# Kernel tuning notes

Measured on AMD Instinct MI355X. Metric: run time of the kernel, lower is better.

Reference implementation:

```python
import jax, jax.numpy as jnp
import numpy as np

N_HEADS, D_K, D_MODEL = 16, 64, 1024
B, S = 2, 2048


def setup_inputs() -> dict:
    key = jax.random.key(0)
    ks = jax.random.split(key, 9)
    scale = 1.0 / np.sqrt(D_MODEL)
    cscale = 1.0 / np.sqrt(N_HEADS * D_K)
    return {
        "x": jax.random.normal(ks[0], (B, S, D_MODEL), dtype=jnp.float32),
        # per-head projection weights, stacked over heads: [H, d_model, d_k]
        "Wq": jax.random.uniform(ks[1], (N_HEADS, D_MODEL, D_K), jnp.float32, -scale, scale),
        "bq": jax.random.uniform(ks[2], (N_HEADS, D_K), jnp.float32, -scale, scale),
        "Wk": jax.random.uniform(ks[3], (N_HEADS, D_MODEL, D_K), jnp.float32, -scale, scale),
        "bk": jax.random.uniform(ks[4], (N_HEADS, D_K), jnp.float32, -scale, scale),
        "Wv": jax.random.uniform(ks[5], (N_HEADS, D_MODEL, D_K), jnp.float32, -scale, scale),
        "bv": jax.random.uniform(ks[6], (N_HEADS, D_K), jnp.float32, -scale, scale),
        # concat projection: [H*d_k, d_model]
        "Wc": jax.random.uniform(ks[7], (N_HEADS * D_K, D_MODEL), jnp.float32, -cscale, cscale),
        "bc": jax.random.uniform(ks[8], (D_MODEL,), jnp.float32, -cscale, cscale),
    }


def reference(x, Wq, bq, Wk, bk, Wv, bv, Wc, bc):
    # Per-head projections, vectorized across heads: [B,H,S,d_k]
    q = jnp.einsum("bsd,hdk->bhsk", x, Wq) + bq[None, :, None, :]
    k = jnp.einsum("bsd,hdk->bhsk", x, Wk) + bk[None, :, None, :]
    v = jnp.einsum("bsd,hdk->bhsk", x, Wv) + bv[None, :, None, :]
    # scores: [B,H,Sq,Skv]
    scores = jnp.einsum("bhsk,bhtk->bhst", q, k) / jnp.sqrt(jnp.asarray(D_K, x.dtype))
    # FAITHFUL to original: softmax over dim=1 of [B,S,S] = the QUERY axis (axis 2 here)
    attn = jax.nn.softmax(scores, axis=2)
    out = jnp.einsum("bhst,bhtk->bhsk", attn, v)  # [B,H,S,d_k]
    # concat heads along feature dim: [B,S,H*d_k]
    cat = jnp.transpose(out, (0, 2, 1, 3)).reshape(x.shape[0], x.shape[1], -1)
    return cat @ Wc + bc
```

## Files before the change

### kernel.cpp

```cpp
#include <hip/hip_runtime.h>
#include <hip/hip_bf16.h>

#define NH 16
#define DK 64
#define DM 1024
#define BB 2
#define SS 2048
#define BS (BB*SS)

typedef __attribute__((ext_vector_type(8))) short bf16x8;
typedef __attribute__((ext_vector_type(4))) short short4v;
typedef __attribute__((ext_vector_type(4))) float f32x4;

#define MFMA16 __builtin_amdgcn_mfma_f32_16x16x32_bf16

static __device__ __forceinline__ f32x4 MFMA16K16(short4v a, short4v b, f32x4 c) {
#if __has_builtin(__builtin_amdgcn_mfma_f32_16x16x16bf16_1k)
  return __builtin_amdgcn_mfma_f32_16x16x16bf16_1k(a, b, c, 0, 0, 0);
#else
  asm volatile("v_mfma_f32_16x16x16_bf16 %0, %1, %2, %0" : "+v"(c) : "v"(a), "v"(b));
  return c;
#endif
}

#if __has_builtin(__builtin_amdgcn_exp2f)
#define EXP2(x) __builtin_amdgcn_exp2f(x)
#else
#define EXP2(x) __expf((x) * 0.6931471805599453f)
#endif

static __device__ __forceinline__ float bf2f(short s) {
  union { unsigned u; float f; } v;
  v.u = ((unsigned)(unsigned short)s) << 16;
  return v.f;
}
static __device__ __forceinline__ short f2bf(float f) {
  union { float f; unsigned u; } v; v.f = f;
  unsigned r = (v.u + 0x7fffu + ((v.u >> 16) & 1u)) >> 16;
  return (short)r;
}
static __device__ __forceinline__ unsigned pkbf(float a, float b) {
  __hip_bfloat162 h = __float22bfloat162_rn(make_float2(a, b));
  union { __hip_bfloat162 h; unsigned u; } c; c.h = h; return c.u;
}

template<int C16>
static __device__ __forceinline__ int soff(int row, int chunk) {
  return row*(C16*8) + ((chunk ^ (row & (C16-1))) << 3);
}

template<int C16, int R>
static __device__ __forceinline__ void stage(const short* __restrict__ g, int gstride,
                                             short* l, int wave, int lane) {
  const int rloc = lane / C16;
  const int c    = lane % C16;
#pragma unroll
  for (int rr = 0; rr < R; rr += 4*(64/C16)) {
    int rbase = rr + wave*(64/C16);
    int row   = rbase + rloc;
    int cg    = c ^ (row & (C16-1));
    __builtin_amdgcn_global_load_lds(
        (const __attribute__((address_space(1))) void*)(g + (size_t)row*gstride + cg*8),
        (__attribute__((address_space(3))) void*)(l + rbase*(C16*8)),
        16, 0, 0);
  }
}

__global__ __launch_bounds__(256) void k_convert(
    const float* __restrict__ x,
    const float* __restrict__ Wq, const float* __restrict__ Wk,
    const float* __restrict__ Wv, const float* __restrict__ Wc,
    short* __restrict__ xb, short* __restrict__ Wt, short* __restrict__ Wct) {
  __shared__ float T[64][65];
  const int tid = threadIdx.x;
  int bx = blockIdx.x;
  const int XB = BS*DM/(256*4);
  if (bx < XB) {
    int i = (bx*256 + tid)*4;
    float4 v = *(const float4*)&x[i];
    union { unsigned u[2]; short4v s; } o;
    o.u[0] = pkbf(v.x, v.y); o.u[1] = pkbf(v.z, v.w);
    *(short4v*)&xb[i] = o.s;
    return;
  }
  bx -= XB;
  if (bx < 48*16) {
    int th = bx >> 4, d0 = (bx & 15) * 64;
    int type = th >> 4, h = th & 15;
    const float* W = ((type == 0) ? Wq : (type == 1) ? Wk : Wv)
                     + (size_t)h*DM*DK + (size_t)d0*DK;
#pragma unroll
    for (int p = 0; p < 4; p++) {
      int dr = p*16 + (tid >> 4), dkc = (tid & 15) * 4;
      float4 v = *(const float4*)&W[(size_t)dr*DK + dkc];
      T[dkc+0][dr]=v.x; T[dkc+1][dr]=v.y; T[dkc+2][dr]=v.z; T[dkc+3][dr]=v.w;
    }
    __syncthreads();
#pragma unroll
    for (int e = 0; e < 2; e++) {
      int c = tid*2 + e, dk = c >> 3, dd = (c & 7) * 8;
      union { short s[8]; int4 v; } u;
#pragma unroll
      for (int j = 0; j < 8; j++) u.s[j] = f2bf(T[dk][dd+j]);
      *(int4*)&Wt[((size_t)th*DK + dk)*DM + d0 + dd] = u.v;
    }
    return;
  }
  bx -= 48*16;
  int n0 = (bx >> 4) * 64, k0 = (bx & 15) * 64;
#pragma unroll
  for (int p = 0; p < 4; p++) {
    int kr = p*16 + (tid >> 4), nc = (tid & 15) * 4;
    float4 v = *(const float4*)&Wc[(size_t)(k0+kr)*DM + n0 + nc];
    T[nc+0][kr]=v.x; T[nc+1][kr]=v.y; T[nc+2][kr]=v.z; T[nc+3][kr]=v.w;
  }
  __syncthreads();
#pragma unroll
  for (int e = 0; e < 2; e++) {
    int c = tid*2 + e, n = c >> 3, kk = (c & 7) * 8;
    union { short s[8]; int4 v; } u;
#pragma unroll
    for (int j = 0; j < 8; j++) u.s[j] = f2bf(T[n][kk+j]);
    *(int4*)&Wct[(size_t)(n0+n)*DM + k0 + kk] = u.v;
  }
}

__global__ __launch_bounds__(256) void k_qkv(
    const short* __restrict__ xb, const short* __restrict__ Wt,
    const float* __restrict__ bq, const float* __restrict__ bk,
    const float* __restrict__ bv,
    short* __restrict__ Qb, short* __restrict__ Kb, short* __restrict__ Vb) {
  __shared__ __align__(16) short As[128*64];
  __shared__ __align__(16) short Bs[128*64];
  const int tid = threadIdx.x, wave = tid >> 6, lane = tid & 63;
  const int l15 = lane & 15, quad = lane >> 4;
  const int id = blockIdx.x, xcd = id & 7, j = id >> 3;
  const int m0 = (xcd*4 + (j & 3)) * 128, n0 = (j >> 2) * 128;
  const int mw = (wave & 1) * 64, nw = (wave >> 1) * 64;
  f32x4 acc[4][4] = {};
  for (int k0 = 0; k0 < DM; k0 += 64) {
    stage<8,128>(xb + (size_t)m0*DM + k0, DM, As, wave, lane);
    stage<8,128>(Wt + (size_t)n0*DM + k0, DM, Bs, wave, lane);
    __syncthreads();
#pragma unroll
    for (int ks = 0; ks < 2; ks++) {
      bf16x8 a[4], b[4];
#pragma unroll
      for (int g = 0; g < 4; g++)  a[g]  = *(const bf16x8*)&As[soff<8>(mw + g*16 + l15,  ks*4 + quad)];
#pragma unroll
      for (int nf = 0; nf < 4; nf++) b[nf] = *(const bf16x8*)&Bs[soff<8>(nw + nf*16 + l15, ks*4 + quad)];
#pragma unroll
      for (int g = 0; g < 4; g++)
#pragma unroll
        for (int nf = 0; nf < 4; nf++)
          acc[g][nf] = MFMA16(a[g], b[nf], acc[g][nf], 0, 0, 0);
    }
    __syncthreads();
  }
  const int th = (n0 + nw) >> 6;
  const int type = th >> 4, h = th & 15;
  short* dst = (type == 0) ? Qb : (type == 1) ? Kb : Vb;
  const float* bias = ((type == 0) ? bq : (type == 1) ? bk : bv) + h*DK;
  const float scale = (type == 0) ? 0.18033688011112042f : 1.0f;
#pragma unroll
  for (int nf = 0; nf < 4; nf++) {
    int dk = nf*16 + l15;
    float bval = bias[dk];
#pragma unroll
    for (int g = 0; g < 4; g++)
#pragma unroll
      for (int r = 0; r < 4; r++) {
        int m = m0 + mw + g*16 + quad*4 + r;
        int b_ = m >> 11, s = m & (SS-1);
        dst[(size_t)((b_*NH + h)*SS + s)*DK + dk] = f2bf((acc[g][nf][r] + bval) * scale);
      }
  }
}

__global__ __launch_bounds__(256) void k_stats(
    const short* __restrict__ Qb, const short* __restrict__ Kb,
    const short* __restrict__ Vb, short* __restrict__ Vt) {
  __shared__ __align__(16) short smem[3*8192];
  __shared__ float red[4][64];
  __shared__ float zinv[128];
  short* Ks = smem;
  const int tid = threadIdx.x, wave = tid >> 6, lane = tid & 63;
  const int l15 = lane & 15, quad = lane >> 4;
  const int id = blockIdx.x, xcd = id & 7, j = id >> 3;
  const int bh = xcd*4 + (j & 3), t0 = (j >> 2) * 128;
  const short* Qg = Qb + (size_t)bh * SS * DK;
  const short* Kg = Kb + (size_t)bh * SS * DK;
  const int mw = (wave & 1) * 64, nw = (wave >> 1) * 64;
  stage<8,128>(Kg + (size_t)t0*DK, DK, Ks, wave, lane);
  stage<8,128>(Qg, DK, smem + 8192, wave, lane);
  __syncthreads();
  bf16x8 kf[2][4];
#pragma unroll
  for (int ks = 0; ks < 2; ks++)
#pragma unroll
    for (int nf = 0; nf < 4; nf++)
      kf[ks][nf] = *(const bf16x8*)&Ks[soff<8>(nw + nf*16 + l15, ks*4 + quad)];
  float csum[4] = {0.f, 0.f, 0.f, 0.f};
  for (int it = 0; it < SS/128; it++) {
    if (it + 1 < SS/128)
      stage<8,128>(Qg + (size_t)(it+1)*128*DK, DK,
                   smem + 8192 + (((it+1) & 1) << 13), wave, lane);
    const short* Qs = smem + 8192 + ((it & 1) << 13);
    f32x4 acc[4][4] = {};
#pragma unroll
    for (int ks = 0; ks < 2; ks++) {
      bf16x8 a[4];
#pragma unroll
      for (int g = 0; g < 4; g++) a[g] = *(const bf16x8*)&Qs[soff<8>(mw + g*16 + l15, ks*4 + quad)];
#pragma unroll
      for (int g = 0; g < 4; g++)
#pragma unroll
        for (int nf = 0; nf < 4; nf++)
          acc[g][nf] = MFMA16(a[g], kf[ks][nf], acc[g][nf], 0, 0, 0);
    }
#pragma unroll
    for (int nf = 0; nf < 4; nf++)
#pragma unroll
      for (int g = 0; g < 4; g++)
#pragma unroll
        for (int r = 0; r < 4; r++)
          csum[nf] += EXP2(acc[g][nf][r]);
    __syncthreads();
  }
#pragma unroll
  for (int nf = 0; nf < 4; nf++) {
    csum[nf] += __shfl_xor(csum[nf], 16, 64);
    csum[nf] += __shfl_xor(csum[nf], 32, 64);
  }
  if (lane < 16) {
#pragma unroll
    for (int nf = 0; nf < 4; nf++) red[wave][nf*16 + lane] = csum[nf];
  }
  __syncthreads();
  if (tid < 128) {
    int half = tid >> 6, c = tid & 63;
    zinv[tid] = 1.0f / (red[half*2][c] + red[half*2 + 1][c]);
  }
  __syncthreads();
  short* Vtile = smem + 8192;
  const short* Vg = Vb + (size_t)bh * SS * DK;
#pragma unroll
  for (int it = 0; it < 4; it++) {
    int c = tid + it*256;
    int trow = c >> 3, c8 = (c & 7) * 8;
    union { int4 v; short s[8]; } u;
    u.v = *(const int4*)&Vg[(size_t)(t0 + trow)*DK + c8];
    float sc = zinv[trow];
#pragma unroll
    for (int jj = 0; jj < 8; jj++) {
      int dk = c8 + jj;
      Vtile[dk*128 + (((trow >> 3) ^ (dk & 15)) << 3) + (trow & 7)] = f2bf(bf2f(u.s[jj]) * sc);
    }
  }
  __syncthreads();
  short* Vtg = Vt + (size_t)bh * DK * SS;
#pragma unroll
  for (int it = 0; it < 4; it++) {
    int row = it*16 + (tid >> 4), cc = tid & 15;
    *(int4*)&Vtg[(size_t)row*SS + t0 + cc*8] = *(const int4*)&Vtile[soff<16>(row, cc)];
  }
}

__global__ __launch_bounds__(256, 2) void k_attnpv(
    const short* __restrict__ Qb, const short* __restrict__ Kb,
    const short* __restrict__ Vt, short* __restrict__ catg) {
  __shared__ __align__(16) short smem[32768];
  const int tid = threadIdx.x, wave = tid >> 6, lane = tid & 63;
  const int l15 = lane & 15, quad = lane >> 4;
  const int id = blockIdx.x, xcd = id & 7, jj = id >> 3;
  const int bh = xcd*4 + (jj & 3), s0 = (jj >> 2) * 128;
  const int b = bh >> 4, h = bh & 15;
  const short* Qg  = Qb + (size_t)bh * SS * DK;
  const short* Kg  = Kb + (size_t)bh * SS * DK;
  const short* Vtg = Vt + (size_t)bh * DK * SS;
  const int th_ = wave & 1, sh = wave >> 1;
  stage<8,128>(Qg + (size_t)s0*DK, DK, smem + 8192, wave, lane);
  stage<8,128>(Kg, DK, smem, wave, lane);
  stage<16,64>(Vtg, SS, smem + 16384, wave, lane);
  __syncthreads();
  bf16x8 qf[2][4];
#pragma unroll
  for (int ks = 0; ks < 2; ks++)
#pragma unroll
    for (int nf = 0; nf < 4; nf++)
      qf[ks][nf] = *(const bf16x8*)&smem[8192 + soff<8>(sh*64 + nf*16 + l15, ks*4 + quad)];
  __syncthreads();
  f32x4 out[4][4] = {};
  for (int it = 0; it < SS/128; it++) {
    const short* Ks = smem + ((it & 1) << 13);
    const short* Vs = smem + 16384 + ((it & 1) << 13);
    f32x4 sacc[4][4] = {};
#pragma unroll
    for (int ks = 0; ks < 2; ks++) {
      bf16x8 a[4];
#pragma unroll
      for (int g = 0; g < 4; g++)
        a[g] = *(const bf16x8*)&Ks[soff<8>(th_*64 + g*16 + l15, ks*4 + quad)];
#pragma unroll
      for (int g = 0; g < 4; g++)
#pragma unroll
        for (int nf = 0; nf < 4; nf++)
          sacc[g][nf] = MFMA16(a[g], qf[ks][nf], sacc[g][nf], 0, 0, 0);
    }
    short4v pa[4][4];
#pragma unroll
    for (int g = 0; g < 4; g++)
#pragma unroll
      for (int nf = 0; nf < 4; nf++) {
        union { unsigned u[2]; short4v s; } pu;
        pu.u[0] = pkbf(EXP2(sacc[g][nf][0]), EXP2(sacc[g][nf][1]));
        pu.u[1] = pkbf(EXP2(sacc[g][nf][2]), EXP2(sacc[g][nf][3]));
        pa[nf][g] = pu.s;
      }
    if (it + 1 < SS/128) {
      stage<8,128>(Kg + (size_t)(it+1)*128*DK, DK, smem + (((it+1) & 1) << 13), wave, lane);
      stage<16,64>(Vtg + (it+1)*128, SS, smem + 16384 + (((it+1) & 1) << 13), wave, lane);
    }
#pragma unroll
    for (int g = 0; g < 4; g++) {
      short4v vb[4];
#pragma unroll
      for (int nv = 0; nv < 4; nv++) {
        int row = nv*16 + l15;
        int ct = (8*th_ + 2*g + (quad >> 1)) ^ (row & 15);
        vb[nv] = *(const short4v*)&Vs[row*128 + (ct << 3) + ((quad & 1) << 2)];
      }
#pragma unroll
      for (int nf = 0; nf < 4; nf++)
#pragma unroll
        for (int nv = 0; nv < 4; nv++)
          out[nf][nv] = MFMA16K16(pa[nf][g], vb[nv], out[nf][nv]);
    }
    __syncthreads();
  }
  float* Pf = (float*)smem;
  if (th_) {
#pragma unroll
    for (int nf = 0; nf < 4; nf++)
#pragma unroll
      for (int nv = 0; nv < 4; nv++)
#pragma unroll
        for (int r = 0; r < 4; r++)
          Pf[sh*4096 + (nf*16 + quad*4 + r)*64 + nv*16 + l15] = out[nf][nv][r];
  }
  __syncthreads();
  if (!th_) {
#pragma unroll
    for (int nf = 0; nf < 4; nf++)
#pragma unroll
      for (int nv = 0; nv < 4; nv++)
#pragma unroll
        for (int r = 0; r < 4; r++) {
          float v = out[nf][nv][r] + Pf[sh*4096 + (nf*16 + quad*4 + r)*64 + nv*16 + l15];
          int s = s0 + sh*64 + nf*16 + quad*4 + r;
          catg[(size_t)(b*SS + s)*DM + h*DK + nv*16 + l15] = f2bf(v);
        }
  }
}

__global__ __launch_bounds__(256) void k_final(
    const short* __restrict__ catg, const short* __restrict__ Wct,
    const float* __restrict__ bc, float* __restrict__ out) {
  __shared__ __align__(16) short As[128*64];
  __shared__ __align__(16) short Bs[128*64];
  const int tid = threadIdx.x, wave = tid >> 6, lane = tid & 63;
  const int l15 = lane & 15, quad = lane >> 4;
  const int id = blockIdx.x, xcd = id & 7, j = id >> 3;
  const int m0 = (xcd*4 + (j & 3)) * 128, n0 = (j >> 2) * 128;
  const int mw = (wave & 1) * 64, nw = (wave >> 1) * 64;
  f32x4 acc[4][4] = {};
  for (int k0 = 0; k0 < DM; k0 += 64) {
    stage<8,128>(catg + (size_t)m0*DM + k0, DM, As, wave, lane);
    stage<8,128>(Wct  + (size_t)n0*DM + k0, DM, Bs, wave, lane);
    __syncthreads();
#pragma unroll
    for (int ks = 0; ks < 2; ks++) {
      bf16x8 a[4], b[4];
#pragma unroll
      for (int g = 0; g < 4; g++)  a[g]  = *(const bf16x8*)&As[soff<8>(mw + g*16 + l15,  ks*4 + quad)];
#pragma unroll
      for (int nf = 0; nf < 4; nf++) b[nf] = *(const bf16x8*)&Bs[soff<8>(nw + nf*16 + l15, ks*4 + quad)];
#pragma unroll
      for (int g = 0; g < 4; g++)
#pragma unroll
        for (int nf = 0; nf < 4; nf++)
          acc[g][nf] = MFMA16(a[g], b[nf], acc[g][nf], 0, 0, 0);
    }
    __syncthreads();
  }
#pragma unroll
  for (int nf = 0; nf < 4; nf++) {
    int n = n0 + nw + nf*16 + l15;
    float bval = bc[n];
#pragma unroll
    for (int g = 0; g < 4; g++)
#pragma unroll
      for (int r = 0; r < 4; r++) {
        int m = m0 + mw + g*16 + quad*4 + r;
        out[(size_t)m*DM + n] = acc[g][nf][r] + bval;
      }
  }
}

extern "C" void kernel_launch(void* const* d_in, const int* in_sizes, int n_in,
                              void* d_out, int out_size, void* d_ws, size_t ws_size,
                              hipStream_t stream) {
  (void)in_sizes; (void)n_in; (void)out_size; (void)ws_size;
  const float* x  = (const float*)d_in[0];
  const float* Wq = (const float*)d_in[1];
  const float* bq = (const float*)d_in[2];
  const float* Wk = (const float*)d_in[3];
  const float* bk = (const float*)d_in[4];
  const float* Wv = (const float*)d_in[5];
  const float* bv = (const float*)d_in[6];
  const float* Wc = (const float*)d_in[7];
  const float* bc = (const float*)d_in[8];
  float* out = (float*)d_out;

  char* ws = (char*)d_ws;
  size_t o = 0;
  short* xb  = (short*)(ws + o); o += (size_t)BS*DM*2;
  short* Wt  = (short*)(ws + o); o += (size_t)3*NH*DK*DM*2;
  short* Wct = (short*)(ws + o); o += (size_t)DM*DM*2;
  short* Qb  = (short*)(ws + o); o += (size_t)BB*NH*SS*DK*2;
  short* Kb  = (short*)(ws + o); o += (size_t)BB*NH*SS*DK*2;
  short* Vb  = (short*)(ws + o); o += (size_t)BB*NH*SS*DK*2;
  short* Vt  = (short*)(ws + o); o += (size_t)BB*NH*DK*SS*2;
  short* cat = (short*)(ws + o); o += (size_t)BS*DM*2;

  const int nconv = BS*DM/(256*4) + 48*16 + 256;
  k_convert<<<dim3(nconv), 256, 0, stream>>>(x, Wq, Wk, Wv, Wc, xb, Wt, Wct);
  k_qkv   <<<dim3(768), 256, 0, stream>>>(xb, Wt, bq, bk, bv, Qb, Kb, Vb);
  k_stats <<<dim3(512), 256, 0, stream>>>(Qb, Kb, Vb, Vt);
  k_attnpv<<<dim3(512), 256, 0, stream>>>(Qb, Kb, Vt, cat);
  k_final <<<dim3(256), 256, 0, stream>>>(cat, Wct, bc, out);
}
```

Before: 220.1 us.

## Use K=32 MFMA for PV via permuted K staging; coalesce QKV stores through LDS

In the attention kernel, K rows are staged into LDS with a row permutation so the exp'd score fragments line up with the 16x16x32 bf16 MFMA layout. The PV product then runs with 8-element bf16 operands, half as many MFMA instructions as the 16x16x16 path, and reads V with wider 16-byte LDS loads. Separately, the QKV projection epilogue writes results into a padded LDS tile and then issues row-contiguous 16-byte global stores instead of scattered 2-byte stores. The risks are wrong results if the permutation does not match the MFMA fragment layout, and an extra sync plus LDS round trip in the projection kernel.

After: 220.2 us. No clear change (+0.1%).

```diff
diff --git a/kernel.cpp b/kernel.cpp
--- a/kernel.cpp
+++ b/kernel.cpp
@@ -13,15 +13,6 @@
 typedef __attribute__((ext_vector_type(4))) float f32x4;
 
 #define MFMA16 __builtin_amdgcn_mfma_f32_16x16x32_bf16
-
-static __device__ __forceinline__ f32x4 MFMA16K16(short4v a, short4v b, f32x4 c) {
-#if __has_builtin(__builtin_amdgcn_mfma_f32_16x16x16bf16_1k)
-  return __builtin_amdgcn_mfma_f32_16x16x16bf16_1k(a, b, c, 0, 0, 0);
-#else
-  asm volatile("v_mfma_f32_16x16x16_bf16 %0, %1, %2, %0" : "+v"(c) : "v"(a), "v"(b));
-  return c;
-#endif
-}
 
 #if __has_builtin(__builtin_amdgcn_exp2f)
 #define EXP2(x) __builtin_amdgcn_exp2f(x)
@@ -62,6 +53,26 @@
     __builtin_amdgcn_global_load_lds(
         (const __attribute__((address_space(1))) void*)(g + (size_t)row*gstride + cg*8),
         (__attribute__((address_space(3))) void*)(l + rbase*(C16*8)),
+        16, 0, 0);
+  }
+}
+
+static __device__ __forceinline__ int permK(int r) {
+  return ((r >> 5) << 5) | ((((r >> 2) & 3)) << 3) | (((r >> 4) & 1) << 2) | (r & 3);
+}
+template<int R>
+static __device__ __forceinline__ void stageP(const short* __restrict__ g, int gstride,
+                                              short* l, int wave, int lane) {
+  const int rloc = lane >> 3;
+  const int c    = lane & 7;
+#pragma unroll
+  for (int rr = 0; rr < R; rr += 32) {
+    int rbase = rr + wave*8;
+    int row   = rbase + rloc;
+    int cg    = c ^ (row & 7);
+    __builtin_amdgcn_global_load_lds(
+        (const __attribute__((address_space(1))) void*)(g + (size_t)permK(row)*gstride + cg*8),
+        (__attribute__((address_space(3))) void*)(l + rbase*64),
         16, 0, 0);
   }
 }
@@ -130,8 +141,9 @@
     const float* __restrict__ bq, const float* __restrict__ bk,
     const float* __restrict__ bv,
     short* __restrict__ Qb, short* __restrict__ Kb, short* __restrict__ Vb) {
-  __shared__ __align__(16) short As[128*64];
-  __shared__ __align__(16) short Bs[128*64];
+  __shared__ __align__(16) short smem[128*130];
+  short* As = smem;
+  short* Bs = smem + 8192;
   const int tid = threadIdx.x, wave = tid >> 6, lane = tid & 63;
   const int l15 = lane & 15, quad = lane >> 4;
   const int id = blockIdx.x, xcd = id & 7, j = id >> 3;
@@ -159,22 +171,29 @@
   }
   const int th = (n0 + nw) >> 6;
   const int type = th >> 4, h = th & 15;
-  short* dst = (type == 0) ? Qb : (type == 1) ? Kb : Vb;
   const float* bias = ((type == 0) ? bq : (type == 1) ? bk : bv) + h*DK;
   const float scale = (type == 0) ? 0.18033688011112042f : 1.0f;
 #pragma unroll
   for (int nf = 0; nf < 4; nf++) {
-    int dk = nf*16 + l15;
-    float bval = bias[dk];
+    float bval = bias[nf*16 + l15];
 #pragma unroll
     for (int g = 0; g < 4; g++)
 #pragma unroll
-      for (int r = 0; r < 4; r++) {
-        int m = m0 + mw + g*16 + quad*4 + r;
-        int b_ = m >> 11, s = m & (SS-1);
-        dst[(size_t)((b_*NH + h)*SS + s)*DK + dk] = f2bf((acc[g][nf][r] + bval) * scale);
-      }
-  }
+      for (int r = 0; r < 4; r++)
+        smem[(mw + g*16 + quad*4 + r)*130 + nw + nf*16 + l15] =
+            f2bf((acc[g][nf][r] + bval) * scale);
+  }
+  __syncthreads();
+  const int row = tid >> 1, half = tid & 1;
+  const int th2 = (n0 >> 6) + half;
+  const int type2 = th2 >> 4, h2 = th2 & 15;
+  short* dst = (type2 == 0) ? Qb : (type2 == 1) ? Kb : Vb;
+  const int m = m0 + row, b_ = m >> 11, s = m & (SS-1);
+  short* drow = dst + (size_t)((b_*NH + h2)*SS + s)*DK;
+  const short* crow = smem + row*130 + half*64;
+#pragma unroll
+  for (int c8 = 0; c8 < 8; c8++)
+    *(int4*)&drow[c8*8] = *(const int4*)&crow[c8*8];
 }
 
 __global__ __launch_bounds__(256) void k_stats(
@@ -280,7 +299,7 @@
   const short* Vtg = Vt + (size_t)bh * DK * SS;
   const int th_ = wave & 1, sh = wave >> 1;
   stage<8,128>(Qg + (size_t)s0*DK, DK, smem + 8192, wave, lane);
-  stage<8,128>(Kg, DK, smem, wave, lane);
+  stageP<128>(Kg, DK, smem, wave, lane);
   stage<16,64>(Vtg, SS, smem + 16384, wave, lane);
   __syncthreads();
   bf16x8 qf[2][4];
@@ -307,34 +326,33 @@
         for (int nf = 0; nf < 4; nf++)
           sacc[g][nf] = MFMA16(a[g], qf[ks][nf], sacc[g][nf], 0, 0, 0);
     }
-    short4v pa[4][4];
-#pragma unroll
-    for (int g = 0; g < 4; g++)
+    bf16x8 pa[4][2];
+#pragma unroll
+    for (int G = 0; G < 2; G++)
 #pragma unroll
       for (int nf = 0; nf < 4; nf++) {
-        union { unsigned u[2]; short4v s; } pu;
-        pu.u[0] = pkbf(EXP2(sacc[g][nf][0]), EXP2(sacc[g][nf][1]));
-        pu.u[1] = pkbf(EXP2(sacc[g][nf][2]), EXP2(sacc[g][nf][3]));
-        pa[nf][g] = pu.s;
+        union { unsigned u[4]; bf16x8 s8; } pu;
+        pu.u[0] = pkbf(EXP2(sacc[2*G][nf][0]),   EXP2(sacc[2*G][nf][1]));
+        pu.u[1] = pkbf(EXP2(sacc[2*G][nf][2]),   EXP2(sacc[2*G][nf][3]));
+        pu.u[2] = pkbf(EXP2(sacc[2*G+1][nf][0]), EXP2(sacc[2*G+1][nf][1]));
+        pu.u[3] = pkbf(EXP2(sacc[2*G+1][nf][2]), EXP2(sacc[2*G+1][nf][3]));
+        pa[nf][G] = pu.s8;
       }
     if (it + 1 < SS/128) {
-      stage<8,128>(Kg + (size_t)(it+1)*128*DK, DK, smem + (((it+1) & 1) << 13), wave, lane);
+      stageP<128>(Kg + (size_t)(it+1)*128*DK, DK, smem + (((it+1) & 1) << 13), wave, lane);
       stage<16,64>(Vtg + (it+1)*128, SS, smem + 16384 + (((it+1) & 1) << 13), wave, lane);
     }
 #pragma unroll
-    for (int g = 0; g < 4; g++) {
-      short4v vb[4];
-#pragma unroll
-      for (int nv = 0; nv < 4; nv++) {
-        int row = nv*16 + l15;
-        int ct = (8*th_ + 2*g + (quad >> 1)) ^ (row & 15);
-        vb[nv] = *(const short4v*)&Vs[row*128 + (ct << 3) + ((quad & 1) << 2)];
-      }
+    for (int G = 0; G < 2; G++) {
+      bf16x8 vb[4];
+#pragma unroll
+      for (int nv = 0; nv < 4; nv++)
+        vb[nv] = *(const bf16x8*)&Vs[soff<16>(nv*16 + l15, 8*th_ + 4*G + quad)];
 #pragma unroll
       for (int nf = 0; nf < 4; nf++)
 #pragma unroll
         for (int nv = 0; nv < 4; nv++)
-          out[nf][nv] = MFMA16K16(pa[nf][g], vb[nv], out[nf][nv]);
+          out[nf][nv] = MFMA16(pa[nf][G], vb[nv], out[nf][nv], 0, 0, 0);
     }
     __syncthreads();
   }
```
